# Kernel optimization log

Hardware: AMD Instinct MI355X
Metric: run time of the kernel (lower is better)

The kernel has to match this reference:

```python
import jax, jax.numpy as jnp
import numpy as np

N_NODES = 100000
N_EDGES = 1600000
FEAT = 128
HID = 128
CLASSES = 10
GRAPHS = 64


def gcn_conv(x, W, b, src, dst, n):
    # PyG GCNConv: h = x @ W; add self-loops; symmetric deg^{-1/2} norm; scatter-add; + bias
    h = x @ W
    src_f = jnp.concatenate([src, jnp.arange(n, dtype=src.dtype)])
    dst_f = jnp.concatenate([dst, jnp.arange(n, dtype=dst.dtype)])
    deg = jax.ops.segment_sum(jnp.ones_like(dst_f, dtype=h.dtype), dst_f, num_segments=n)
    dinv = jax.lax.rsqrt(jnp.where(deg > 0, deg, 1.0))
    norm = dinv[src_f] * dinv[dst_f]              # [E+N]
    msg = h[src_f] * norm[:, None]                # gather + scale
    out = jax.ops.segment_sum(msg, dst_f, num_segments=n)  # scatter-add
    return out + b


def global_mean_pool(x, batch, num_graphs):
    s = jax.ops.segment_sum(x, batch, num_segments=num_graphs)
    cnt = jax.ops.segment_sum(jnp.ones_like(batch, dtype=x.dtype), batch, num_segments=num_graphs)
    return s / jnp.maximum(cnt, 1.0)[:, None]


def setup_inputs() -> dict:
    key = jax.random.key(0)
    ks = jax.random.split(key, 10)
    x = jax.random.normal(ks[0], (N_NODES, FEAT), dtype=jnp.float32)
    edge_index = jax.random.randint(ks[1], (2, N_EDGES), 0, N_NODES, dtype=jnp.int64)
    batch = jnp.sort(jax.random.randint(ks[2], (N_NODES,), 0, GRAPHS, dtype=jnp.int64))
    def glorot(k, fi, fo):
        s = float(np.sqrt(6.0 / (fi + fo)))
        return jax.random.uniform(k, (fi, fo), jnp.float32, -s, s)
    return {
        "x": x, "edge_index": edge_index, "batch": batch,
        "W1": glorot(ks[3], FEAT, HID), "b1": jnp.zeros((HID,), jnp.float32),
        "W2": glorot(ks[4], HID, HID), "b2": jnp.zeros((HID,), jnp.float32),
        "W3": glorot(ks[5], HID, HID), "b3": jnp.zeros((HID,), jnp.float32),
        "Wlin": glorot(ks[6], HID, CLASSES), "blin": jnp.zeros((CLASSES,), jnp.float32),
    }


def reference(x, edge_index, batch, W1, b1, W2, b2, W3, b3, Wlin, blin):
    src, dst = edge_index[0], edge_index[1]
    n = x.shape[0]
    h = jax.nn.relu(gcn_conv(x, W1, b1, src, dst, n))
    h = jax.nn.relu(gcn_conv(h, W2, b2, src, dst, n))
    h = gcn_conv(h, W3, b3, src, dst, n)
    emb = global_mean_pool(h, batch, GRAPHS)      # [GRAPHS, HID]
    # dropout(p=0.5) is identity in eval mode
    logits = emb @ Wlin + blin                    # [GRAPHS, CLASSES]
    return logits, jnp.squeeze(emb)
```

## Files before the change

### kernel.cpp

```cpp
#include <hip/hip_runtime.h>
#include <hip/hip_bf16.h>
#include <stdint.h>

typedef unsigned int uint32;
typedef __attribute__((ext_vector_type(8))) short short8;
typedef __attribute__((ext_vector_type(4))) float float4v;
typedef __attribute__((ext_vector_type(2))) float f32x2;

#define FEAT 128
#define NGRAPH 64
#define GB   256
#define NBK  512

__device__ __forceinline__ float bf2f_lo(uint32 v) {
    union { uint32 i; float f; } u; u.i = v << 16; return u.f;
}
__device__ __forceinline__ float bf2f_hi(uint32 v) {
    union { uint32 i; float f; } u; u.i = v & 0xffff0000u; return u.f;
}
__device__ __forceinline__ unsigned short f2bf(float f) {
    uint32 u = __builtin_bit_cast(uint32, f);
    uint32 r = (u + 0x7fffu + ((u >> 16) & 1u)) >> 16;
    return (unsigned short)r;
}
__device__ __forceinline__ uint32 f2bf2(float lo, float hi) {
    return (uint32)f2bf(lo) | ((uint32)f2bf(hi) << 16);
}

__global__ void k_wswz(const float* __restrict__ W1, const float* __restrict__ W2,
                       const float* __restrict__ W3, unsigned short* __restrict__ o1,
                       unsigned short* __restrict__ o2, unsigned short* __restrict__ o3,
                       int* __restrict__ cursor, int CAP) {
    int t = threadIdx.x, blk = blockIdx.x;
    if (blk == 0)
        for (int b = t; b < NBK; b += 256) cursor[b] = b * CAP;
    int wid = blk >> 3;
    const float* W = (wid == 0) ? W1 : (wid == 1) ? W2 : W3;
    unsigned short* out = (wid == 0) ? o1 : (wid == 1) ? o2 : o3;
    int e = (blk & 7) * 256 + t;
    int kt = e >> 9, ct = (e >> 6) & 7, lane = e & 63;
    int krow = kt * 32 + (lane >> 4) * 8;
    int col = ct * 16 + (lane & 15);
#pragma unroll
    for (int j = 0; j < 8; j++)
        out[e * 8 + j] = f2bf(W[(krow + j) * FEAT + col]);
}

__global__ void k_bscat2(const int* __restrict__ src, const int* __restrict__ dst,
                         int* __restrict__ cursor, uint32* __restrict__ ebuf, int E) {
    __shared__ int h[NBK];
    __shared__ int cur[NBK];
    int t = threadIdx.x, blk = blockIdx.x;
    for (int b = t; b < NBK; b += 256) h[b] = 0;
    __syncthreads();
    int chunk = (E + GB - 1) / GB;
    int lo = blk * chunk, hi = min(lo + chunk, E);
    for (int e = lo + t; e < hi; e += 256)
        atomicAdd(&h[dst[e] >> 8], 1);
    __syncthreads();
    for (int b = t; b < NBK; b += 256) {
        int c = h[b];
        cur[b] = c ? atomicAdd(&cursor[b], c) : 0;
    }
    __syncthreads();
    for (int e = lo + t; e < hi; e += 256) {
        int d = dst[e], s = src[e];
        int p = atomicAdd(&cur[d >> 8], 1);
        ebuf[p] = ((uint32)s << 8) | (uint32)(d & 255);
    }
}

__global__ void k_csr2(const uint32* __restrict__ ebuf, const int* __restrict__ cursor,
                       float* __restrict__ dinv, int2* __restrict__ rowp2,
                       int* __restrict__ csrc, int N, int CAP) {
    __shared__ int h[256];
    __shared__ int cur[256];
    int t = threadIdx.x, b = blockIdx.x;
    int e0 = b * CAP;
    int e1 = cursor[b];
    h[t] = 0;
    __syncthreads();
    for (int e = e0 + t; e < e1; e += 256)
        atomicAdd(&h[ebuf[e] & 255u], 1);
    __syncthreads();
    int deg = h[t];
    cur[t] = deg;
    __syncthreads();
    for (int off = 1; off < 256; off <<= 1) {
        int v = (t >= off) ? cur[t - off] : 0;
        __syncthreads();
        cur[t] += v;
        __syncthreads();
    }
    int r = e0 + cur[t] - deg;
    int node = b * 256 + t;
    if (node < N) {
        rowp2[node] = make_int2(r, r + deg);
        dinv[node] = rsqrtf((float)deg + 1.0f);
    }
    cur[t] = r;
    __syncthreads();
    for (int e = e0 + t; e < e1; e += 256) {
        uint32 v = ebuf[e];
        int p = atomicAdd(&cur[v & 255u], 1);
        csrc[p] = (int)(v >> 8);
    }
}

template <bool F32IN>
__global__ void k_gemm(const void* __restrict__ Xp,
                       const unsigned short* __restrict__ Wswz,
                       const float* __restrict__ dinv,
                       unsigned short* __restrict__ Hb, int N) {
    __shared__ unsigned short Wl[FEAT * FEAT];
    {
        const uint4* Wg = (const uint4*)Wswz;
        uint4* Ws = (uint4*)Wl;
        for (int i = threadIdx.x; i < 2048; i += 256) Ws[i] = Wg[i];
    }
    __syncthreads();

    int wave = threadIdx.x >> 6, lane = threadIdx.x & 63;
    int r0 = (blockIdx.x * 4 + wave) * 16;
    if (r0 >= N) return;
    int m = lane & 15, q = lane >> 4;

    int arow = r0 + m; if (arow >= N) arow = N - 1;
    short8 a[4];
    if (F32IN) {
        const float* Ar = (const float*)Xp + (long)arow * FEAT;
#pragma unroll
        for (int kt = 0; kt < 4; kt++) {
            float4 u = *(const float4*)(Ar + kt * 32 + q * 8);
            float4 v = *(const float4*)(Ar + kt * 32 + q * 8 + 4);
            short8 tv;
            tv[0] = (short)f2bf(u.x); tv[1] = (short)f2bf(u.y);
            tv[2] = (short)f2bf(u.z); tv[3] = (short)f2bf(u.w);
            tv[4] = (short)f2bf(v.x); tv[5] = (short)f2bf(v.y);
            tv[6] = (short)f2bf(v.z); tv[7] = (short)f2bf(v.w);
            a[kt] = tv;
        }
    } else {
        const short8* Ar = (const short8*)((const unsigned short*)Xp + (long)arow * FEAT);
#pragma unroll
        for (int kt = 0; kt < 4; kt++) a[kt] = Ar[kt * 4 + q];
    }

    const short8* Bl = (const short8*)Wl;
    float4v acc[8];
#pragma unroll
    for (int ct = 0; ct < 8; ct++) acc[ct] = (float4v){0.f, 0.f, 0.f, 0.f};
#pragma unroll
    for (int ct = 0; ct < 8; ct++) {
        acc[ct] = __builtin_amdgcn_mfma_f32_16x16x32_bf16(Bl[(0 * 8 + ct) * 64 + lane], a[0], acc[ct], 0, 0, 0);
        acc[ct] = __builtin_amdgcn_mfma_f32_16x16x32_bf16(Bl[(1 * 8 + ct) * 64 + lane], a[1], acc[ct], 0, 0, 0);
        acc[ct] = __builtin_amdgcn_mfma_f32_16x16x32_bf16(Bl[(2 * 8 + ct) * 64 + lane], a[2], acc[ct], 0, 0, 0);
        acc[ct] = __builtin_amdgcn_mfma_f32_16x16x32_bf16(Bl[(3 * 8 + ct) * 64 + lane], a[3], acc[ct], 0, 0, 0);
    }

    int node = r0 + m;
    bool ok = (node < N);
    float d = ok ? dinv[node] : 0.f;
#pragma unroll
    for (int ct = 0; ct < 8; ct++) {
        if (ok) {
            uint2 o;
            o.x = f2bf2(acc[ct][0] * d, acc[ct][1] * d);
            o.y = f2bf2(acc[ct][2] * d, acc[ct][3] * d);
            ((uint2*)(Hb + (long)node * FEAT + ct * 16))[q] = o;
        }
    }
}

template <int RELU>
__global__ void k_agg(const uint32* __restrict__ Hb,
                      const int2* __restrict__ rowp2, const int* __restrict__ csrc,
                      const float* __restrict__ dinv, const float* __restrict__ bias,
                      uint32* __restrict__ OUTb, int N) {
    int wave = threadIdx.x >> 6, lane = threadIdx.x & 63;
    int i = blockIdx.x * 4 + wave;
    if (i >= N) return;
    int f = lane & 15, quarter = lane >> 4;
    const uint4* H4 = (const uint4*)Hb;
    f32x2 c0 = {0.f, 0.f}, c1 = c0, c2 = c0, c3 = c0;
    int2 rr = rowp2[i];
    int e0 = rr.x, e1 = rr.y;
    int e = e0;
    for (; e + 16 <= e1; e += 16) {
        int  s[4];
        uint4 h[4];
#pragma unroll
        for (int j = 0; j < 4; j++) s[j] = csrc[e + 4 * j + quarter];
#pragma unroll
        for (int j = 0; j < 4; j++) h[j] = H4[(long)s[j] * 16 + f];
#pragma unroll
        for (int j = 0; j < 4; j++) {
            f32x2 u;
            u.x = bf2f_lo(h[j].x); u.y = bf2f_hi(h[j].x); c0 += u;
            u.x = bf2f_lo(h[j].y); u.y = bf2f_hi(h[j].y); c1 += u;
            u.x = bf2f_lo(h[j].z); u.y = bf2f_hi(h[j].z); c2 += u;
            u.x = bf2f_lo(h[j].w); u.y = bf2f_hi(h[j].w); c3 += u;
        }
    }
    {
        int r = e1 - e;
        int  s[4];
        uint4 h[4];
#pragma unroll
        for (int j = 0; j < 4; j++) {
            int idx = 4 * j + quarter;
            if (idx < r) s[j] = csrc[e + idx];
        }
#pragma unroll
        for (int j = 0; j < 4; j++)
            if (4 * j + quarter < r) h[j] = H4[(long)s[j] * 16 + f];
#pragma unroll
        for (int j = 0; j < 4; j++)
            if (4 * j + quarter < r) {
                f32x2 u;
                u.x = bf2f_lo(h[j].x); u.y = bf2f_hi(h[j].x); c0 += u;
                u.x = bf2f_lo(h[j].y); u.y = bf2f_hi(h[j].y); c1 += u;
                u.x = bf2f_lo(h[j].z); u.y = bf2f_hi(h[j].z); c2 += u;
                u.x = bf2f_lo(h[j].w); u.y = bf2f_hi(h[j].w); c3 += u;
            }
    }
    c0.x += __shfl_xor(c0.x, 16); c0.y += __shfl_xor(c0.y, 16);
    c1.x += __shfl_xor(c1.x, 16); c1.y += __shfl_xor(c1.y, 16);
    c2.x += __shfl_xor(c2.x, 16); c2.y += __shfl_xor(c2.y, 16);
    c3.x += __shfl_xor(c3.x, 16); c3.y += __shfl_xor(c3.y, 16);
    c0.x += __shfl_xor(c0.x, 32); c0.y += __shfl_xor(c0.y, 32);
    c1.x += __shfl_xor(c1.x, 32); c1.y += __shfl_xor(c1.y, 32);
    c2.x += __shfl_xor(c2.x, 32); c2.y += __shfl_xor(c2.y, 32);
    c3.x += __shfl_xor(c3.x, 32); c3.y += __shfl_xor(c3.y, 32);
    if (quarter == 0) {
        uint4 hv = H4[(long)i * 16 + f];
        c0.x += bf2f_lo(hv.x); c0.y += bf2f_hi(hv.x);
        c1.x += bf2f_lo(hv.y); c1.y += bf2f_hi(hv.y);
        c2.x += bf2f_lo(hv.z); c2.y += bf2f_hi(hv.z);
        c3.x += bf2f_lo(hv.w); c3.y += bf2f_hi(hv.w);
        float di = dinv[i];
        const float4* b4 = (const float4*)bias;
        float4 bb0 = b4[2 * f], bb1 = b4[2 * f + 1];
        c0.x = c0.x * di + bb0.x; c0.y = c0.y * di + bb0.y;
        c1.x = c1.x * di + bb0.z; c1.y = c1.y * di + bb0.w;
        c2.x = c2.x * di + bb1.x; c2.y = c2.y * di + bb1.y;
        c3.x = c3.x * di + bb1.z; c3.y = c3.y * di + bb1.w;
        if (RELU) {
            c0.x = fmaxf(c0.x, 0.f); c0.y = fmaxf(c0.y, 0.f);
            c1.x = fmaxf(c1.x, 0.f); c1.y = fmaxf(c1.y, 0.f);
            c2.x = fmaxf(c2.x, 0.f); c2.y = fmaxf(c2.y, 0.f);
            c3.x = fmaxf(c3.x, 0.f); c3.y = fmaxf(c3.y, 0.f);
        }
        uint4 o;
        o.x = f2bf2(c0.x, c0.y);
        o.y = f2bf2(c1.x, c1.y);
        o.z = f2bf2(c2.x, c2.y);
        o.w = f2bf2(c3.x, c3.y);
        ((uint4*)OUTb)[(long)i * 16 + f] = o;
    }
}

__global__ void k_pf(const uint32* __restrict__ Gb, const int* __restrict__ batch,
                     const float* __restrict__ Wlin, const float* __restrict__ blin,
                     float* __restrict__ out, int N) {
    __shared__ float spx[1024], spy[1024];
    __shared__ float es[FEAT];
    int t = threadIdx.x, g = blockIdx.x;
    int lo, hi;
    { int l = 0, h = N; while (l < h) { int m = (l + h) >> 1; if (batch[m] < g) l = m + 1; else h = m; } lo = l; }
    { int l = lo, h = N; while (l < h) { int m = (l + h) >> 1; if (batch[m] < g + 1) l = m + 1; else h = m; } hi = l; }
    int f = t & 63, sub = t >> 6;
    float ax = 0.f, ay = 0.f;
#pragma unroll 4
    for (int i = lo + sub; i < hi; i += 16) {
        uint32 v = Gb[(long)i * 64 + f];
        ax += bf2f_lo(v); ay += bf2f_hi(v);
    }
    spx[t] = ax; spy[t] = ay;
    __syncthreads();
    if (t < 64) {
        float sx = 0.f, sy = 0.f;
#pragma unroll
        for (int r = 0; r < 16; r++) { sx += spx[t + 64 * r]; sy += spy[t + 64 * r]; }
        float c = (float)max(hi - lo, 1);
        float e0 = sx / c, e1 = sy / c;
        es[2 * t] = e0; es[2 * t + 1] = e1;
        out[NGRAPH * 10 + g * FEAT + 2 * t]     = e0;
        out[NGRAPH * 10 + g * FEAT + 2 * t + 1] = e1;
    }
    __syncthreads();
    if (t < 10) {
        float a = blin[t];
        for (int k = 0; k < FEAT; k++)
            a += es[k] * Wlin[k * 10 + t];
        out[g * 10 + t] = a;
    }
}

extern "C" void kernel_launch(void* const* d_in, const int* in_sizes, int n_in,
                              void* d_out, int out_size, void* d_ws, size_t ws_size,
                              hipStream_t stream) {
    const float* x    = (const float*)d_in[0];
    const int*   ei   = (const int*)d_in[1];
    const int*   batch= (const int*)d_in[2];
    const float* W1   = (const float*)d_in[3];
    const float* b1   = (const float*)d_in[4];
    const float* W2   = (const float*)d_in[5];
    const float* b2   = (const float*)d_in[6];
    const float* W3   = (const float*)d_in[7];
    const float* b3   = (const float*)d_in[8];
    const float* Wlin = (const float*)d_in[9];
    const float* blin = (const float*)d_in[10];

    const int N = in_sizes[2];
    const int E = in_sizes[1] / 2;
    const int* src = ei;
    const int* dst = ei + E;
    const int NB = (N + 255) >> 8;
    int CAP = ((E * 2 / (NB > 0 ? NB : 1)) + 255) & ~255;
    if (CAP < 1024) CAP = 1024;

    char* w = (char*)d_ws;
    auto take = [&](size_t bytes) {
        char* p = w;
        w += (bytes + 255) & ~(size_t)255;
        return p;
    };
    float*  dinv   = (float*) take((size_t)N * 4);
    int2*   rowp2  = (int2*)  take((size_t)N * 8);
    int*    csrc   = (int*)   take((size_t)NB * CAP * 4);
    uint32* ebuf   = (uint32*)take((size_t)NB * CAP * 4);
    int*    cursor = (int*)   take((size_t)NBK * 4);
    uint32* hbuf   = (uint32*)take((size_t)N * FEAT * 2);
    uint32* gbuf   = (uint32*)take((size_t)N * FEAT * 2);
    unsigned short* w1s = (unsigned short*)take(FEAT * FEAT * 2);
    unsigned short* w2s = (unsigned short*)take(FEAT * FEAT * 2);
    unsigned short* w3s = (unsigned short*)take(FEAT * FEAT * 2);
    (void)ws_size; (void)n_in; (void)out_size;

    k_wswz  <<<24, 256, 0, stream>>>(W1, W2, W3, w1s, w2s, w3s, cursor, CAP);
    k_bscat2<<<GB, 256, 0, stream>>>(src, dst, cursor, ebuf, E);
    k_csr2  <<<NB, 256, 0, stream>>>(ebuf, cursor, dinv, rowp2, csrc, N, CAP);

    const int tile_blocks = (N + 63) / 64;
    const int agg_blocks  = (N + 3) / 4;

    k_gemm<true> <<<tile_blocks, 256, 0, stream>>>(x, w1s, dinv, (unsigned short*)hbuf, N);
    k_agg<1><<<agg_blocks, 256, 0, stream>>>(hbuf, rowp2, csrc, dinv, b1, gbuf, N);
    k_gemm<false><<<tile_blocks, 256, 0, stream>>>(gbuf, w2s, dinv, (unsigned short*)hbuf, N);
    k_agg<1><<<agg_blocks, 256, 0, stream>>>(hbuf, rowp2, csrc, dinv, b2, gbuf, N);
    k_gemm<false><<<tile_blocks, 256, 0, stream>>>(gbuf, w3s, dinv, (unsigned short*)hbuf, N);
    k_agg<0><<<agg_blocks, 256, 0, stream>>>(hbuf, rowp2, csrc, dinv, b3, gbuf, N);

    k_pf<<<NGRAPH, 1024, 0, stream>>>(gbuf, batch, Wlin, blin, (float*)d_out, N);
}
```

Baseline: 394.0 us.

## Fuse weight swizzle into bucket scatter, widen preprocessing grids, split pooling

```diff
diff --git a/kernel.cpp b/kernel.cpp
--- a/kernel.cpp
+++ b/kernel.cpp
@@ -9,8 +9,9 @@
 
 #define FEAT 128
 #define NGRAPH 64
-#define GB   256
+#define GB2  1024
 #define NBK  512
+#define QPG  8
 
 __device__ __forceinline__ float bf2f_lo(uint32 v) {
     union { uint32 i; float f; } u; u.i = v << 16; return u.f;
@@ -27,40 +28,39 @@
     return (uint32)f2bf(lo) | ((uint32)f2bf(hi) << 16);
 }
 
-__global__ void k_wswz(const float* __restrict__ W1, const float* __restrict__ W2,
-                       const float* __restrict__ W3, unsigned short* __restrict__ o1,
-                       unsigned short* __restrict__ o2, unsigned short* __restrict__ o3,
-                       int* __restrict__ cursor, int CAP) {
+__global__ void k_bscat2(const int* __restrict__ src, const int* __restrict__ dst,
+                         int* __restrict__ cursor, uint32* __restrict__ ebuf, int E,
+                         const float* __restrict__ W1, const float* __restrict__ W2,
+                         const float* __restrict__ W3, unsigned short* __restrict__ o1,
+                         unsigned short* __restrict__ o2, unsigned short* __restrict__ o3,
+                         int CAP) {
     int t = threadIdx.x, blk = blockIdx.x;
-    if (blk == 0)
-        for (int b = t; b < NBK; b += 256) cursor[b] = b * CAP;
-    int wid = blk >> 3;
-    const float* W = (wid == 0) ? W1 : (wid == 1) ? W2 : W3;
-    unsigned short* out = (wid == 0) ? o1 : (wid == 1) ? o2 : o3;
-    int e = (blk & 7) * 256 + t;
-    int kt = e >> 9, ct = (e >> 6) & 7, lane = e & 63;
-    int krow = kt * 32 + (lane >> 4) * 8;
-    int col = ct * 16 + (lane & 15);
-#pragma unroll
-    for (int j = 0; j < 8; j++)
-        out[e * 8 + j] = f2bf(W[(krow + j) * FEAT + col]);
-}
-
-__global__ void k_bscat2(const int* __restrict__ src, const int* __restrict__ dst,
-                         int* __restrict__ cursor, uint32* __restrict__ ebuf, int E) {
+    if (blk >= GB2) {
+        int b2 = blk - GB2;
+        int wid = b2 >> 3;
+        const float* W = (wid == 0) ? W1 : (wid == 1) ? W2 : W3;
+        unsigned short* out = (wid == 0) ? o1 : (wid == 1) ? o2 : o3;
+        int e = (b2 & 7) * 256 + t;
+        int kt = e >> 9, ct = (e >> 6) & 7, lane = e & 63;
+        int krow = kt * 32 + (lane >> 4) * 8;
+        int col = ct * 16 + (lane & 15);
+#pragma unroll
+        for (int j = 0; j < 8; j++)
+            out[e * 8 + j] = f2bf(W[(krow + j) * FEAT + col]);
+        return;
+    }
     __shared__ int h[NBK];
     __shared__ int cur[NBK];
-    int t = threadIdx.x, blk = blockIdx.x;
     for (int b = t; b < NBK; b += 256) h[b] = 0;
     __syncthreads();
-    int chunk = (E + GB - 1) / GB;
+    int chunk = (E + GB2 - 1) / GB2;
     int lo = blk * chunk, hi = min(lo + chunk, E);
     for (int e = lo + t; e < hi; e += 256)
         atomicAdd(&h[dst[e] >> 8], 1);
     __syncthreads();
     for (int b = t; b < NBK; b += 256) {
         int c = h[b];
-        cur[b] = c ? atomicAdd(&cursor[b], c) : 0;
+        cur[b] = c ? (b * CAP + atomicAdd(&cursor[b], c)) : 0;
     }
     __syncthreads();
     for (int e = lo + t; e < hi; e += 256) {
@@ -77,30 +77,36 @@
     __shared__ int cur[256];
     int t = threadIdx.x, b = blockIdx.x;
     int e0 = b * CAP;
-    int e1 = cursor[b];
-    h[t] = 0;
-    __syncthreads();
-    for (int e = e0 + t; e < e1; e += 256)
+    int e1 = e0 + cursor[b];
+    if (t < 256) h[t] = 0;
+    __syncthreads();
+    for (int e = e0 + t; e < e1; e += 512)
         atomicAdd(&h[ebuf[e] & 255u], 1);
     __syncthreads();
-    int deg = h[t];
-    cur[t] = deg;
+    int deg = 0;
+    if (t < 256) {
+        deg = h[t];
+        cur[t] = deg;
+    }
     __syncthreads();
     for (int off = 1; off < 256; off <<= 1) {
-        int v = (t >= off) ? cur[t - off] : 0;
+        int v = 0;
+        if (t < 256 && t >= off) v = cur[t - off];
         __syncthreads();
-        cur[t] += v;
+        if (t < 256) cur[t] += v;
         __syncthreads();
     }
-    int r = e0 + cur[t] - deg;
-    int node = b * 256 + t;
-    if (node < N) {
-        rowp2[node] = make_int2(r, r + deg);
-        dinv[node] = rsqrtf((float)deg + 1.0f);
-    }
-    cur[t] = r;
-    __syncthreads();
-    for (int e = e0 + t; e < e1; e += 256) {
+    if (t < 256) {
+        int r = e0 + cur[t] - deg;
+        int node = b * 256 + t;
+        if (node < N) {
+            rowp2[node] = make_int2(r, r + deg);
+            dinv[node] = rsqrtf((float)deg + 1.0f);
+        }
+        cur[t] = r;
+    }
+    __syncthreads();
+    for (int e = e0 + t; e < e1; e += 512) {
         uint32 v = ebuf[e];
         int p = atomicAdd(&cur[v & 255u], 1);
         csrc[p] = (int)(v >> 8);
@@ -260,34 +266,59 @@
     }
 }
 
-__global__ void k_pf(const uint32* __restrict__ Gb, const int* __restrict__ batch,
-                     const float* __restrict__ Wlin, const float* __restrict__ blin,
-                     float* __restrict__ out, int N) {
-    __shared__ float spx[1024], spy[1024];
-    __shared__ float es[FEAT];
-    int t = threadIdx.x, g = blockIdx.x;
+__global__ void k_pool2(const uint32* __restrict__ Gb, const int* __restrict__ batch,
+                        float* __restrict__ pool, int N) {
+    __shared__ float spx[256], spy[256];
+    int t = threadIdx.x;
+    int g = blockIdx.x >> 3, qtr = blockIdx.x & (QPG - 1);
     int lo, hi;
     { int l = 0, h = N; while (l < h) { int m = (l + h) >> 1; if (batch[m] < g) l = m + 1; else h = m; } lo = l; }
     { int l = lo, h = N; while (l < h) { int m = (l + h) >> 1; if (batch[m] < g + 1) l = m + 1; else h = m; } hi = l; }
+    int cnt = hi - lo;
+    int chunk = (cnt + QPG - 1) / QPG;
+    int lo2 = lo + qtr * chunk;
+    int hi2 = min(lo2 + chunk, hi);
     int f = t & 63, sub = t >> 6;
     float ax = 0.f, ay = 0.f;
 #pragma unroll 4
-    for (int i = lo + sub; i < hi; i += 16) {
+    for (int i = lo2 + sub; i < hi2; i += 4) {
         uint32 v = Gb[(long)i * 64 + f];
         ax += bf2f_lo(v); ay += bf2f_hi(v);
     }
     spx[t] = ax; spy[t] = ay;
     __syncthreads();
     if (t < 64) {
-        float sx = 0.f, sy = 0.f;
-#pragma unroll
-        for (int r = 0; r < 16; r++) { sx += spx[t + 64 * r]; sy += spy[t + 64 * r]; }
-        float c = (float)max(hi - lo, 1);
-        float e0 = sx / c, e1 = sy / c;
-        es[2 * t] = e0; es[2 * t + 1] = e1;
-        out[NGRAPH * 10 + g * FEAT + 2 * t]     = e0;
-        out[NGRAPH * 10 + g * FEAT + 2 * t + 1] = e1;
-    }
+        float sx = spx[t] + spx[t + 64] + spx[t + 128] + spx[t + 192];
+        float sy = spy[t] + spy[t + 64] + spy[t + 128] + spy[t + 192];
+        float* pr = pool + ((size_t)qtr * NGRAPH + g) * FEAT;
+        pr[2 * t]     = sx;
+        pr[2 * t + 1] = sy;
+    }
+}
+
+__global__ void k_final(const float* __restrict__ pool, const int* __restrict__ batch,
+                        const float* __restrict__ Wlin, const float* __restrict__ blin,
+                        float* __restrict__ out, int N) {
+    __shared__ float es[FEAT];
+    __shared__ int lohi[2];
+    int g = blockIdx.x, t = threadIdx.x;
+    if (t < 2) {
+        int key = g + t;
+        int lo = 0, hi = N;
+        while (lo < hi) {
+            int mid = (lo + hi) >> 1;
+            if (batch[mid] < key) lo = mid + 1; else hi = mid;
+        }
+        lohi[t] = lo;
+    }
+    float s = 0.f;
+#pragma unroll
+    for (int r = 0; r < QPG; r++) s += pool[(r * NGRAPH + g) * FEAT + t];
+    __syncthreads();
+    float c = (float)max(lohi[1] - lohi[0], 1);
+    float e = s / c;
+    es[t] = e;
+    out[NGRAPH * 10 + g * FEAT + t] = e;
     __syncthreads();
     if (t < 10) {
         float a = blin[t];
@@ -336,11 +367,13 @@
     unsigned short* w1s = (unsigned short*)take(FEAT * FEAT * 2);
     unsigned short* w2s = (unsigned short*)take(FEAT * FEAT * 2);
     unsigned short* w3s = (unsigned short*)take(FEAT * FEAT * 2);
+    float*  pool   = (float*) take((size_t)QPG * NGRAPH * FEAT * 4);
     (void)ws_size; (void)n_in; (void)out_size;
 
-    k_wswz  <<<24, 256, 0, stream>>>(W1, W2, W3, w1s, w2s, w3s, cursor, CAP);
-    k_bscat2<<<GB, 256, 0, stream>>>(src, dst, cursor, ebuf, E);
-    k_csr2  <<<NB, 256, 0, stream>>>(ebuf, cursor, dinv, rowp2, csrc, N, CAP);
+    hipMemsetAsync(cursor, 0, NBK * sizeof(int), stream);
+    k_bscat2<<<GB2 + 24, 256, 0, stream>>>(src, dst, cursor, ebuf, E,
+                                           W1, W2, W3, w1s, w2s, w3s, CAP);
+    k_csr2  <<<NB, 512, 0, stream>>>(ebuf, cursor, dinv, rowp2, csrc, N, CAP);
 
     const int tile_blocks = (N + 63) / 64;
     const int agg_blocks  = (N + 3) / 4;
@@ -352,5 +385,6 @@
     k_gemm<false><<<tile_blocks, 256, 0, stream>>>(gbuf, w3s, dinv, (unsigned short*)hbuf, N);
     k_agg<0><<<agg_blocks, 256, 0, stream>>>(hbuf, rowp2, csrc, dinv, b3, gbuf, N);
 
-    k_pf<<<NGRAPH, 1024, 0, stream>>>(gbuf, batch, Wlin, blin, (float*)d_out, N);
-}
+    k_pool2<<<NGRAPH * QPG, 256, 0, stream>>>(gbuf, batch, pool, N);
+    k_final<<<NGRAPH, 128, 0, stream>>>(pool, batch, Wlin, blin, (float*)d_out, N);
+}
```

Result: slower. 415.0 us (+5.3%).
